# Optimization experiments

Hardware: AMD Instinct MI355X
Metric: run time of the kernel (lower is better)

The kernel has to match this reference:

```python
import jax, jax.numpy as jnp
import numpy as np

KH = KW = 3  # deform conv kernel
EPS = 1e-12  # F.normalize eps


def _deform_sample(img, u, v):
    """Flow-guided deformable sampling: bilinear gather of img at each of the
    9 kernel offsets shifted by the per-pixel flow (u=dx, v=dy).
    img: [B,C,H,W]; u,v: [B,1,H,W] -> returns [B,C,9,H,W]."""
    B, C, H, W = img.shape
    ky, kx = jnp.meshgrid(jnp.arange(KH) - 1, jnp.arange(KW) - 1, indexing='ij')
    ky = ky.reshape(1, 9, 1, 1).astype(img.dtype)
    kx = kx.reshape(1, 9, 1, 1).astype(img.dtype)
    iy = jnp.arange(H, dtype=img.dtype).reshape(1, 1, H, 1)
    ix = jnp.arange(W, dtype=img.dtype).reshape(1, 1, 1, W)
    py = iy + ky + v  # [B,9,H,W]
    px = ix + kx + u
    y0 = jnp.floor(py); x0 = jnp.floor(px)
    wy = py - y0; wx = px - x0  # bilinear weights
    y0i = y0.astype(jnp.int32); x0i = x0.astype(jnp.int32)
    flat = img.reshape(B, C, H * W)

    def gather(yi, xi):
        valid = ((yi >= 0) & (yi < H) & (xi >= 0) & (xi < W)).astype(img.dtype)
        idx = jnp.clip(yi, 0, H - 1) * W + jnp.clip(xi, 0, W - 1)  # [B,9,H,W]
        g = jax.vmap(lambda f, i: jnp.take(f, i.reshape(-1), axis=1))(flat, idx)
        return g.reshape(B, C, 9, H, W) * valid[:, None]

    s = (gather(y0i, x0i) * ((1 - wy) * (1 - wx))[:, None]
         + gather(y0i, x0i + 1) * ((1 - wy) * wx)[:, None]
         + gather(y0i + 1, x0i) * (wy * (1 - wx))[:, None]
         + gather(y0i + 1, x0i + 1) * (wy * wx)[:, None])
    return s


def setup_inputs() -> dict:
    key = jax.random.key(0)
    k1, k2, k3, k4, k5 = jax.random.split(key, 5)
    B, C, H, W = 2, 64, 256, 256
    num_heads = 4
    clone = jax.random.normal(k1, (B, C, H, W), dtype=jnp.float32)
    x = jax.random.normal(k2, (B, C, H * W), dtype=jnp.float32)
    u = jax.random.normal(k3, (B, 1, H, W), dtype=jnp.float32)
    v = jax.random.normal(k4, (B, 1, H, W), dtype=jnp.float32)
    weight = jax.random.normal(k5, (C, C, KH, KW), dtype=jnp.float32) * 0.05
    temperature = jnp.ones((num_heads, 1, 1), dtype=jnp.float32)
    return {"clone": clone, "x": x, "u": u, "v": v,
            "weight": weight, "temperature": temperature}


def reference(clone, x, u, v, weight, temperature):
    # deformable conv: bilinear gather then contract over (in_ch, kernel)
    s = _deform_sample(clone, u, v)                      # [B,C,9,H,W]
    w = weight.reshape(weight.shape[0], weight.shape[1], 9)
    conv = jnp.einsum('bckhw,ock->bohw', s, w)           # [B,C,H,W]
    B, C, H, W = conv.shape
    head = temperature.shape[0]
    kv = conv.reshape(B, head, C // head, H * W)          # k = v = deform output
    q = x.reshape(B, head, C // head, H * W)
    qn = q / jnp.maximum(jnp.linalg.norm(q, axis=-1, keepdims=True), EPS)
    kn = kv / jnp.maximum(jnp.linalg.norm(kv, axis=-1, keepdims=True), EPS)
    attn = jnp.einsum('bhcs,bhds->bhcd', qn, kn) * temperature  # [B,h,c,c]
    attn = jax.nn.softmax(attn, axis=-1)
    out = jnp.einsum('bhcd,bhds->bhcs', attn, kv)
    return out.reshape(B, C, H * W)
```

## Files before the change

### kernel.cpp

```cpp
#include <hip/hip_runtime.h>

typedef __bf16 bf16;
typedef __bf16 bf16x4 __attribute__((ext_vector_type(4)));
typedef __bf16 bf16x8 __attribute__((ext_vector_type(8)));
typedef float  f32x2  __attribute__((ext_vector_type(2)));
typedef float  f32x4  __attribute__((ext_vector_type(4)));

#define HH 256
#define WW 256
#define NB 2
#define NC 64
#define NS 65536
#define EX 258
#define NHEAD 4
#define DH 16
#define NSTRIPE 8
#define ACCSZ 2304

#define OFF_CEXT   0ul
#define OFF_KV     17040384ul
#define OFF_WPK    33817600ul
#define OFF_ACC    33891328ul

__global__ void k0w(const float* __restrict__ wgt, bf16* __restrict__ wpk,
                    float* __restrict__ accums) {
    int t = blockIdx.x * 256 + threadIdx.x;
    if (t < 9 * 2 * 4 * 64) {
        int L   = t & 63;
        int mtg = (t >> 6) & 3;
        int kc  = (t >> 8) & 1;
        int tap = t >> 9;
        int o  = mtg * 16 + (L & 15);
        int cb = kc * 32 + (L >> 4) * 8;
        bf16x8 vv;
        #pragma unroll
        for (int j = 0; j < 8; j++)
            vv[j] = (bf16)wgt[(o * 64 + (cb + j)) * 9 + tap];
        *(bf16x8*)(wpk + t * 8) = vv;
    }
    int z = t - 9 * 2 * 4 * 64;
    if (z >= 0 && z < NSTRIPE * ACCSZ) accums[z] = 0.0f;
}

__global__ __launch_bounds__(256, 2) void k1_conv(const float* __restrict__ clone,
                                                  const bf16* __restrict__ wpk,
                                                  bf16* __restrict__ cext) {
    const int Xt = blockIdx.x;
    const int Yt = blockIdx.y;
    const int b  = blockIdx.z;
    const int t  = threadIdx.x;
    const int L  = t & 63;
    const int wv = t >> 6;
    const int mpair = wv >> 1;
    const int npair = wv & 1;

    extern __shared__ bf16 tile[];

    bf16x8 afrag[2][9][2];
    #pragma unroll
    for (int mt = 0; mt < 2; mt++)
        #pragma unroll
        for (int tap = 0; tap < 9; tap++)
            #pragma unroll
            for (int kc = 0; kc < 2; kc++) {
                int idx = ((tap * 2 + kc) * 4 + (mpair * 2 + mt)) * 64 + L;
                afrag[mt][tap][kc] = *(const bf16x8*)(wpk + idx * 8);
            }

    for (int u = t; u < 2176; u += 256) {
        int xq = u % 17;
        int rc = u / 17;
        int cg = rc & 15;
        int r  = rc >> 4;
        int y  = Yt * 6 - 2 + r;
        int xg0 = Xt * 64 - 4 + xq * 4;
        int c0 = cg * 4;
        f32x4 f[4];
        bool yin = (y >= 0) && (y < HH);
        if (yin && xg0 >= 0 && xg0 + 3 < WW) {
            #pragma unroll
            for (int i = 0; i < 4; i++)
                f[i] = *(const f32x4*)(clone + ((size_t)(b * NC + c0 + i) * HH + y) * WW + xg0);
        } else {
            #pragma unroll
            for (int i = 0; i < 4; i++)
                #pragma unroll
                for (int e = 0; e < 4; e++) {
                    int xg = xg0 + e;
                    f[i][e] = (yin && xg >= 0 && xg < WW)
                            ? clone[((size_t)(b * NC + c0 + i) * HH + y) * WW + xg] : 0.0f;
                }
        }
        #pragma unroll
        for (int e = 0; e < 4; e++) {
            bf16x4 h;
            #pragma unroll
            for (int i = 0; i < 4; i++) h[i] = (bf16)f[i][e];
            *(bf16x4*)(tile + (r * 68 + xq * 4 + e) * 72 + c0) = h;
        }
    }
    __syncthreads();

    const int nbase = Xt * 64 + npair * 32;
    const f32x4 zero4 = {0.0f, 0.0f, 0.0f, 0.0f};
    for (int Yi = 0; Yi < 6; Yi++) {
        f32x4 acc[2][2];
        acc[0][0] = zero4; acc[0][1] = zero4; acc[1][0] = zero4; acc[1][1] = zero4;
        #pragma unroll
        for (int tap = 0; tap < 9; tap++) {
            const int ky = tap / 3 - 1;
            const int kx = tap % 3 - 1;
            const int r = Yi + 1 + ky;
            #pragma unroll
            for (int kc = 0; kc < 2; kc++) {
                const int cb = kc * 32 + (L >> 4) * 8;
                #pragma unroll
                for (int nt = 0; nt < 2; nt++) {
                    if (nbase + nt * 16 < EX) {
                        const int col = npair * 32 + nt * 16 + (L & 15) + kx + 3;
                        bf16x8 bfrag = *(const bf16x8*)(tile + (r * 68 + col) * 72 + cb);
                        #pragma unroll
                        for (int mt = 0; mt < 2; mt++)
                            acc[mt][nt] = __builtin_amdgcn_mfma_f32_16x16x32_bf16(
                                afrag[mt][tap][kc], bfrag, acc[mt][nt], 0, 0, 0);
                    }
                }
            }
        }
        int Yp = Yt * 6 + Yi;
        #pragma unroll
        for (int mt = 0; mt < 2; mt++)
            #pragma unroll
            for (int nt = 0; nt < 2; nt++) {
                int Xp = Xt * 64 + npair * 32 + nt * 16 + (L & 15);
                if (Xp < EX) {
                    int o = mpair * 32 + mt * 16 + (L >> 4) * 4;
                    bf16x4 st;
                    #pragma unroll
                    for (int rg = 0; rg < 4; rg++) st[rg] = (bf16)acc[mt][nt][rg];
                    *(bf16x4*)(cext + ((((size_t)b * EX + Yp) * EX + Xp) << 6) + o) = st;
                }
            }
    }
}

__global__ __launch_bounds__(256) void k2_gd(const float* __restrict__ uu,
                                             const float* __restrict__ vv,
                                             const float* __restrict__ x,
                                             const bf16* __restrict__ cext,
                                             bf16* __restrict__ kvT,
                                             float* __restrict__ accums) {
    const int bx = blockIdx.x;
    const int b  = blockIdx.z;
    const int strip = (bx & 7) * 128 + (bx >> 3);
    const int t = threadIdx.x;
    const int px = t >> 2;
    const int q4 = t & 3;
    const int hw = strip * 64 + px;
    const int idx = b * NS + hw;
    const int hy = hw >> 8;
    const int wx = hw & 255;

    __shared__ bf16 tile[64][68];

    float fv = vv[idx];
    float fu = uu[idx];
    float py_f = (float)hy + fv;
    float px_f = (float)wx + fu;
    float fy = floorf(py_f);
    float fx = floorf(px_f);
    float ay = py_f - fy;
    float ax = px_f - fx;
    int ys = (int)fy + 1;
    int xs = (int)fx + 1;
    float w00 = (1.0f - ay) * (1.0f - ax);
    float w01 = (1.0f - ay) * ax;
    float w10 = ay * (1.0f - ax);
    float w11 = ay * ax;
    bool y0i = (ys >= 0) && (ys < EX);
    bool y1i = (ys + 1 >= 0) && (ys + 1 < EX);
    bool x0i = (xs >= 0) && (xs < EX);
    bool x1i = (xs + 1 >= 0) && (xs + 1 < EX);
    if (!y0i) { w00 = 0.0f; w01 = 0.0f; }
    if (!y1i) { w10 = 0.0f; w11 = 0.0f; }
    if (!x0i) { w00 = 0.0f; w10 = 0.0f; }
    if (!x1i) { w01 = 0.0f; w11 = 0.0f; }
    int y0c = ys < 0 ? 0 : (ys > EX - 1 ? EX - 1 : ys);
    int y1c = ys + 1 < 0 ? 0 : (ys + 1 > EX - 1 ? EX - 1 : ys + 1);
    int x0c = xs < 0 ? 0 : (xs > EX - 1 ? EX - 1 : xs);
    int x1c = xs + 1 < 0 ? 0 : (xs + 1 > EX - 1 ? EX - 1 : xs + 1);
    const bf16* pb = cext + (((size_t)b * EX * EX) << 6);
    size_t i00 = ((size_t)(y0c * EX + x0c)) << 6;
    size_t i01 = ((size_t)(y0c * EX + x1c)) << 6;
    size_t i10 = ((size_t)(y1c * EX + x0c)) << 6;
    size_t i11 = ((size_t)(y1c * EX + x1c)) << 6;
    const int c0 = q4 * 16;
    bf16* kvp = kvT + ((size_t)(b * NS + hw)) * 64 + c0;
    #pragma unroll
    for (int g = 0; g < 2; g++) {
        int cg = c0 + g * 8;
        bf16x8 c00 = *(const bf16x8*)(pb + i00 + cg);
        bf16x8 c01 = *(const bf16x8*)(pb + i01 + cg);
        bf16x8 c10 = *(const bf16x8*)(pb + i10 + cg);
        bf16x8 c11 = *(const bf16x8*)(pb + i11 + cg);
        bf16x4 lo, hi;
        bf16x8 sv;
        #pragma unroll
        for (int j = 0; j < 8; j++) {
            float val = w00 * (float)c00[j] + w01 * (float)c01[j]
                      + w10 * (float)c10[j] + w11 * (float)c11[j];
            bf16 hv = (bf16)val;
            sv[j] = hv;
            if (j < 4) lo[j] = hv; else hi[j - 4] = hv;
        }
        *(bf16x8*)(kvp + g * 8) = sv;
        *(bf16x4*)(&tile[px][cg])     = lo;
        *(bf16x4*)(&tile[px][cg + 4]) = hi;
    }
    __syncthreads();

    const int L  = t & 63;
    const int h  = t >> 6;
    const int row = L & 15;
    const int kg  = L >> 4;
    const int bh = b * NHEAD + h;
    const float* qb = x + ((size_t)(b * NC + h * DH + row)) * NS + strip * 64;
    f32x4 acc = {0.0f, 0.0f, 0.0f, 0.0f};
    float qp = 0.0f, kp = 0.0f;
    #pragma unroll
    for (int it = 0; it < 2; it++) {
        const int s = it * 32 + kg * 8;
        f32x4 q0 = *(const f32x4*)(qb + s);
        f32x4 q1 = *(const f32x4*)(qb + s + 4);
        bf16x8 qa, ka;
        #pragma unroll
        for (int j = 0; j < 4; j++) {
            qa[j]     = (bf16)q0[j];
            qa[j + 4] = (bf16)q1[j];
        }
        #pragma unroll
        for (int j = 0; j < 8; j++) ka[j] = tile[s + j][h * DH + row];
        qp += q0[0]*q0[0] + q0[1]*q0[1] + q0[2]*q0[2] + q0[3]*q0[3]
            + q1[0]*q1[0] + q1[1]*q1[1] + q1[2]*q1[2] + q1[3]*q1[3];
        #pragma unroll
        for (int j = 0; j < 8; j++) {
            float kf = (float)ka[j];
            kp += kf * kf;
        }
        acc = __builtin_amdgcn_mfma_f32_16x16x32_bf16(qa, ka, acc, 0, 0, 0);
    }
    float* astripe = accums + (bx & 7) * ACCSZ;
    #pragma unroll
    for (int rg = 0; rg < 4; rg++)
        atomicAdd(astripe + bh * 256 + (kg * 4 + rg) * 16 + row, acc[rg]);
    qp += __shfl_xor(qp, 16); qp += __shfl_xor(qp, 32);
    kp += __shfl_xor(kp, 16); kp += __shfl_xor(kp, 32);
    if (kg == 0) {
        atomicAdd(astripe + 2048 + bh * 16 + row, qp);
        atomicAdd(astripe + 2176 + bh * 16 + row, kp);
    }
}

__global__ __launch_bounds__(256) void k5_out(const bf16* __restrict__ kvT,
                                              const float* __restrict__ accums,
                                              const float* __restrict__ temp,
                                              float* __restrict__ out) {
    const int ci = blockIdx.x;
    const int h  = blockIdx.y;
    const int b  = blockIdx.z;
    const int t  = threadIdx.x;
    const int bh = b * NHEAD + h;
    __shared__ float l[256];
    __shared__ float a[256];
    {
        int i = t >> 4, j = t & 15;
        float dsum = 0.0f, q2 = 0.0f, k2 = 0.0f;
        #pragma unroll
        for (int st = 0; st < NSTRIPE; st++) {
            dsum += accums[st * ACCSZ + bh * 256 + t];
            q2   += accums[st * ACCSZ + 2048 + bh * 16 + i];
            k2   += accums[st * ACCSZ + 2176 + bh * 16 + j];
        }
        float qn = fmaxf(sqrtf(q2), 1e-12f);
        float kn = fmaxf(sqrtf(k2), 1e-12f);
        float logit = dsum / (qn * kn) * temp[h];
        l[t] = logit;
        __syncthreads();
        float mx = -1e30f;
        #pragma unroll
        for (int jj = 0; jj < 16; jj++) mx = fmaxf(mx, l[i * 16 + jj]);
        float sum = 0.0f;
        #pragma unroll
        for (int jj = 0; jj < 16; jj++) sum += expf(l[i * 16 + jj] - mx);
        a[t] = expf(logit - mx) / sum;
        __syncthreads();
    }
    const int s = (ci * 256 + t) * 2;
    const bf16* kvb = kvT + ((size_t)(b * NS + s)) * 64 + h * DH;
    f32x2 kf[16];
    #pragma unroll
    for (int e = 0; e < 2; e++) {
        bf16x8 k0 = *(const bf16x8*)(kvb + e * 64);
        bf16x8 k1 = *(const bf16x8*)(kvb + e * 64 + 8);
        #pragma unroll
        for (int j = 0; j < 8; j++) {
            kf[j][e]     = (float)k0[j];
            kf[8 + j][e] = (float)k1[j];
        }
    }
    float* ob = out + ((size_t)(b * NC + h * DH)) * NS + s;
    #pragma unroll
    for (int i = 0; i < 16; i++) {
        f32x2 o = {0.0f, 0.0f};
        #pragma unroll
        for (int j = 0; j < 16; j++)
            o += a[i * 16 + j] * kf[j];
        *(f32x2*)(ob + (size_t)i * NS) = o;
    }
}

extern "C" void kernel_launch(void* const* d_in, const int* in_sizes, int n_in,
                              void* d_out, int out_size, void* d_ws, size_t ws_size,
                              hipStream_t stream) {
    const float* clone = (const float*)d_in[0];
    const float* x     = (const float*)d_in[1];
    const float* u     = (const float*)d_in[2];
    const float* v     = (const float*)d_in[3];
    const float* wgt   = (const float*)d_in[4];
    const float* temp  = (const float*)d_in[5];
    float* out = (float*)d_out;

    char* ws = (char*)d_ws;
    bf16*  cext   = (bf16*) (ws + OFF_CEXT);
    bf16*  kvT    = (bf16*) (ws + OFF_KV);
    bf16*  wpk    = (bf16*) (ws + OFF_WPK);
    float* accums = (float*)(ws + OFF_ACC);

    static bool attr_set = false;
    if (!attr_set) {
        hipFuncSetAttribute((const void*)k1_conv,
                            hipFuncAttributeMaxDynamicSharedMemorySize, 78336);
        attr_set = true;
    }

    k0w<<<90, 256, 0, stream>>>(wgt, wpk, accums);
    k1_conv<<<dim3(5, 43, 2), 256, 78336, stream>>>(clone, wpk, cext);
    k2_gd<<<dim3(1024, 1, 2), 256, 0, stream>>>(u, v, x, cext, kvT, accums);
    k5_out<<<dim3(128, 4, 2), 256, 0, stream>>>(kvT, accums, temp, out);
}
```

Baseline: 156.6 us.

## Compute attention output with bf16 MFMA using hi/lo split weights and remapped blocks

Replaces the scalar FMA loop in the output kernel with a 16x16x32 bf16 MFMA per 16-position chunk. The softmax weights are split into a bf16 high part and a bf16 residual so that their precision is kept across the K dimension. It also permutes the block-to-chunk mapping, so consecutive blocks touch strided positions, which may spread memory traffic. In exchange, output stores become 16-lane 4-byte scattered writes per row rather than vectorized f32x2 stores.

```diff
diff --git a/kernel.cpp b/kernel.cpp
--- a/kernel.cpp
+++ b/kernel.cpp
@@ -265,7 +265,8 @@
                                               const float* __restrict__ accums,
                                               const float* __restrict__ temp,
                                               float* __restrict__ out) {
-    const int ci = blockIdx.x;
+    const int bx = blockIdx.x;
+    const int ci = (bx & 7) * 16 + (bx >> 3);
     const int h  = blockIdx.y;
     const int b  = blockIdx.z;
     const int t  = threadIdx.x;
@@ -295,27 +296,30 @@
         a[t] = expf(logit - mx) / sum;
         __syncthreads();
     }
-    const int s = (ci * 256 + t) * 2;
-    const bf16* kvb = kvT + ((size_t)(b * NS + s)) * 64 + h * DH;
-    f32x2 kf[16];
-    #pragma unroll
-    for (int e = 0; e < 2; e++) {
-        bf16x8 k0 = *(const bf16x8*)(kvb + e * 64);
-        bf16x8 k1 = *(const bf16x8*)(kvb + e * 64 + 8);
-        #pragma unroll
-        for (int j = 0; j < 8; j++) {
-            kf[j][e]     = (float)k0[j];
-            kf[8 + j][e] = (float)k1[j];
-        }
-    }
-    float* ob = out + ((size_t)(b * NC + h * DH)) * NS + s;
-    #pragma unroll
-    for (int i = 0; i < 16; i++) {
-        f32x2 o = {0.0f, 0.0f};
-        #pragma unroll
-        for (int j = 0; j < 16; j++)
-            o += a[i * 16 + j] * kf[j];
-        *(f32x2*)(ob + (size_t)i * NS) = o;
+
+    const int L  = t & 63;
+    const int wv = t >> 6;
+    const int m  = L & 15;
+    const int kg = L >> 4;
+
+    bf16x8 af;
+    #pragma unroll
+    for (int j = 0; j < 8; j++) {
+        float v = a[m * 16 + (kg & 1) * 8 + j];
+        bf16 hv = (bf16)v;
+        af[j] = (kg < 2) ? hv : (bf16)(v - (float)hv);
+    }
+
+    const bf16* kvb = kvT + ((size_t)b * NS) * 64 + h * DH + (kg & 1) * 8;
+    #pragma unroll
+    for (int ch = 0; ch < 8; ch++) {
+        const int s0 = ci * 512 + wv * 128 + ch * 16;
+        bf16x8 kb = *(const bf16x8*)(kvb + (size_t)(s0 + m) * 64);
+        f32x4 acc = {0.0f, 0.0f, 0.0f, 0.0f};
+        acc = __builtin_amdgcn_mfma_f32_16x16x32_bf16(af, kb, acc, 0, 0, 0);
+        #pragma unroll
+        for (int r = 0; r < 4; r++)
+            out[(((size_t)(b * NC + h * DH + kg * 4 + r)) << 16) + s0 + m] = acc[r];
     }
 }
 
```

After: 157.6 us. No clear change (+0.7%).
